# Kernel optimization log

Hardware: AMD Instinct MI355X
Metric: run time of the kernel (lower is better)

## Reference

```python
import jax, jax.numpy as jnp
import numpy as np

BN_EPS = 1e-3  # keras BatchNormalization default epsilon


def setup_inputs() -> dict:
    key = jax.random.key(0)
    ks = jax.random.split(key, 8)
    B, H, W, C, K, CLS = 8, 64, 64, 512, 32, 21
    std = 1.0 / (K * C) ** 0.5
    x = jax.random.normal(ks[0], (B, H, W, C), dtype=jnp.float32)
    codewords = jax.random.uniform(ks[1], (C, K), dtype=jnp.float32, minval=-std, maxval=std)
    smoothing_factors = jax.random.uniform(ks[2], (K,), dtype=jnp.float32, minval=-1.0, maxval=0.0)
    # BatchNormalization(axis=-2) over (B, features, K): per-feature params, inference stats
    bn_gamma = jnp.ones((C,), dtype=jnp.float32)
    bn_beta = jnp.zeros((C,), dtype=jnp.float32)
    bn_mean = jnp.zeros((C,), dtype=jnp.float32)
    bn_var = jnp.ones((C,), dtype=jnp.float32)
    # Dense layers (glorot-uniform style init)
    lim1 = (6.0 / (C + C)) ** 0.5
    w_enc = jax.random.uniform(ks[3], (C, C), dtype=jnp.float32, minval=-lim1, maxval=lim1)
    b_enc = jnp.zeros((C,), dtype=jnp.float32)
    lim2 = (6.0 / (C + CLS)) ** 0.5
    w_se = jax.random.uniform(ks[4], (C, CLS), dtype=jnp.float32, minval=-lim2, maxval=lim2)
    b_se = jnp.zeros((CLS,), dtype=jnp.float32)
    return {"x": x, "codewords": codewords, "smoothing_factors": smoothing_factors,
            "bn_gamma": bn_gamma, "bn_beta": bn_beta, "bn_mean": bn_mean, "bn_var": bn_var,
            "w_enc": w_enc, "b_enc": b_enc, "w_se": w_se, "b_se": b_se}


def _encoder(x, codewords, smoothing_factors, bn_gamma, bn_beta, bn_mean, bn_var):
    B, H, W, C = x.shape
    K = codewords.shape[1]
    N = H * W
    xf = x.reshape(B, N, C)
    # squared residual norms ||x_n - c_k||^2 via expansion (same math as the
    # explicit (B,N,C,K) residual tensor in the original, without materializing it)
    x_sq = jnp.sum(xf * xf, axis=-1, keepdims=True)          # (B,N,1)
    cw_sq = jnp.sum(codewords * codewords, axis=0)            # (K,)
    cross = jnp.einsum('bnc,ck->bnk', xf, codewords)          # (B,N,K)
    sqnorms = x_sq - 2.0 * cross + cw_sq                      # (B,N,K)
    # softmax over codewords of -(sqnorm * smoothing_factor)
    weights = jax.nn.softmax(-(sqnorms * smoothing_factors), axis=-1)  # (B,N,K)
    # sum_n w_nk * (x_n - c_k) = (w^T x)_ck - c_k * sum_n w_nk
    wx = jnp.einsum('bnk,bnc->bck', weights, xf)              # (B,C,K)
    wsum = jnp.sum(weights, axis=1)                           # (B,K)
    enc = wx - codewords[None, :, :] * wsum[:, None, :]       # (B,C,K)
    # BatchNorm(axis=-2) in inference mode: normalize per-feature across (B,K)
    inv = jax.lax.rsqrt(bn_var + BN_EPS)
    enc_bn = (enc - bn_mean[None, :, None]) * (inv * bn_gamma)[None, :, None] + bn_beta[None, :, None]
    enc_relu = jax.nn.relu(enc_bn)
    out = jnp.sum(enc_relu, axis=-1)                          # (B,C)
    return out.reshape(B, 1, 1, C)


def reference(x, codewords, smoothing_factors, bn_gamma, bn_beta, bn_mean, bn_var,
              w_enc, b_enc, w_se, b_se):
    B = x.shape[0]
    C = codewords.shape[0]
    encodings = _encoder(x, codewords, smoothing_factors, bn_gamma, bn_beta, bn_mean, bn_var)  # (B,1,1,C)
    attn = jax.nn.sigmoid(jnp.einsum('bijc,cd->bijd', encodings, w_enc) + b_enc)  # (B,1,1,C)
    featuremaps_output = attn * x                                                  # (B,H,W,C)
    enc_vec = encodings.reshape(B, C)
    se_loss_output = jax.nn.sigmoid(enc_vec @ w_se + b_se)                         # (B,classes)
    return featuremaps_output, se_loss_output
```

## Files before the change

### kernel.cpp

```cpp
#include <hip/hip_runtime.h>

#define BB 8
#define NN 4096
#define CCH 512
#define KK 32
#define CLS 21
#define BN_EPS 1e-3f

#define CHUNK 128
#define NBLK (NN / CHUNK)

typedef _Float16 f16;
typedef _Float16 f16x4 __attribute__((ext_vector_type(4)));
typedef _Float16 f16x8 __attribute__((ext_vector_type(8)));
typedef float f32x4 __attribute__((ext_vector_type(4)));

#define WP 136

#define WS_P    0
#define WS_WSP  (NBLK * BB * CCH * KK / 2)
#define WS_ENC  (WS_WSP + NBLK * BB * KK)
#define WS_END  (WS_ENC + BB * CCH)

template <int CTRL>
__device__ __forceinline__ float dpp_add(float v) {
    int r = __builtin_amdgcn_update_dpp(0, __builtin_bit_cast(int, v),
                                        CTRL, 0xF, 0xF, true);
    return v + __builtin_bit_cast(float, r);
}
template <int CTRL>
__device__ __forceinline__ float dpp_max(float v) {
    int r = __builtin_amdgcn_update_dpp(0, __builtin_bit_cast(int, v),
                                        CTRL, 0xF, 0xF, true);
    return fmaxf(v, __builtin_bit_cast(float, r));
}
__device__ __forceinline__ float rowsum16(float v) {
    v = dpp_add<0x128>(v); v = dpp_add<0x124>(v);
    v = dpp_add<0x122>(v); v = dpp_add<0x121>(v);
    return v;
}
__device__ __forceinline__ float rowmax16(float v) {
    v = dpp_max<0x128>(v); v = dpp_max<0x124>(v);
    v = dpp_max<0x122>(v); v = dpp_max<0x121>(v);
    return v;
}

__global__ __launch_bounds__(512, 2) void enc_mfma(
    const float* __restrict__ x, const float* __restrict__ cw,
    const float* __restrict__ sf, float* __restrict__ ws)
{
    __shared__ f16   cwL[2048 * 8];
    __shared__ f16   wexch[32 * WP];
    __shared__ float wsq[8][KK];
    __shared__ float csqL[KK];
    __shared__ float nsfL[KK];
    __shared__ float redtmp[8][KK];

    const int t = threadIdx.x;
    const int w = t >> 6, l = t & 63, a = l & 15, g = l >> 4;
    const int chunk = blockIdx.x, b = blockIdx.y;
    const int n0 = chunk * CHUNK;

#pragma unroll
    for (int si = 0; si < 4; ++si) {
        const int s     = si * 512 + t;
        const int lane  = s & 63;
        const int cstep = (s >> 6) & 15;
        const int kt    = s >> 10;
        const int k     = (lane & 15) + 16 * kt;
        const int c0    = cstep * 32 + (lane >> 4) * 8;
        f16x8 v;
#pragma unroll
        for (int i = 0; i < 8; ++i) v[i] = (f16)cw[(c0 + i) * KK + k];
        *reinterpret_cast<f16x8*>(cwL + (size_t)s * 8) = v;
    }
    if (t < 256) {
        const int k = t & 31, part = t >> 5;
        float s = 0.f;
        for (int c = part * 64; c < part * 64 + 64; ++c) {
            const float v = cw[c * KK + k];
            s += v * v;
        }
        redtmp[part][k] = s;
    }
    __syncthreads();
    if (t < KK) {
        float s = 0.f;
#pragma unroll
        for (int p = 0; p < 8; ++p) s += redtmp[p][t];
        csqL[t] = s;
        nsfL[t] = -sf[t];
    }
    __syncthreads();

    const float csq0 = csqL[a], csq1 = csqL[a + 16];
    const float nsf0 = nsfL[a], nsf1 = nsfL[a + 16];

    f32x4 d0 = {0.f, 0.f, 0.f, 0.f}, d1 = {0.f, 0.f, 0.f, 0.f};
    float xs = 0.f;
    {
        const float* xrow = x + (size_t)(b * NN + n0 + w * 16 + a) * CCH;
        float4 u0 = *reinterpret_cast<const float4*>(xrow + g * 8);
        float4 u1 = *reinterpret_cast<const float4*>(xrow + g * 8 + 4);
#pragma unroll
        for (int cs = 0; cs < 16; ++cs) {
            float4 p0, p1;
            if (cs < 15) {
                const int cn = (cs + 1) * 32 + g * 8;
                p0 = *reinterpret_cast<const float4*>(xrow + cn);
                p1 = *reinterpret_cast<const float4*>(xrow + cn + 4);
            }
            xs += u0.x*u0.x + u0.y*u0.y + u0.z*u0.z + u0.w*u0.w
                + u1.x*u1.x + u1.y*u1.y + u1.z*u1.z + u1.w*u1.w;
            const f16x8 af = {(f16)u0.x, (f16)u0.y, (f16)u0.z, (f16)u0.w,
                              (f16)u1.x, (f16)u1.y, (f16)u1.z, (f16)u1.w};
            const f16x8 bf0 = *reinterpret_cast<const f16x8*>(
                cwL + ((size_t)cs * 64 + l) * 8);
            const f16x8 bf1 = *reinterpret_cast<const f16x8*>(
                cwL + ((size_t)(16 + cs) * 64 + l) * 8);
            d0 = __builtin_amdgcn_mfma_f32_16x16x32_f16(af, bf0, d0, 0, 0, 0);
            d1 = __builtin_amdgcn_mfma_f32_16x16x32_f16(af, bf1, d1, 0, 0, 0);
            u0 = p0; u1 = p1;
        }
        xs += __shfl_xor(xs, 16);
        xs += __shfl_xor(xs, 32);
    }

    float wsacc0 = 0.f, wsacc1 = 0.f;
#pragma unroll
    for (int r = 0; r < 4; ++r) {
        const int rho = g * 4 + r;
        const float xsr = __shfl(xs, rho);
        const float l0 = (xsr - 2.f * d0[r] + csq0) * nsf0;
        const float l1 = (xsr - 2.f * d1[r] + csq1) * nsf1;
        const float mx = rowmax16(fmaxf(l0, l1));
        const float e0 = __expf(l0 - mx);
        const float e1 = __expf(l1 - mx);
        const float inv = 1.f / rowsum16(e0 + e1);
        const float w0 = e0 * inv, w1 = e1 * inv;
        wsacc0 += w0; wsacc1 += w1;
        wexch[(a     ) * WP + w * 16 + rho] = (f16)w0;
        wexch[(a + 16) * WP + w * 16 + rho] = (f16)w1;
    }
    wsacc0 += __shfl_xor(wsacc0, 16); wsacc0 += __shfl_xor(wsacc0, 32);
    wsacc1 += __shfl_xor(wsacc1, 16); wsacc1 += __shfl_xor(wsacc1, 32);
    if (l < 16) { wsq[w][l] = wsacc0; wsq[w][l + 16] = wsacc1; }

    __syncthreads();

    f32x4 acc[4][2];
#pragma unroll
    for (int ct = 0; ct < 4; ++ct)
#pragma unroll
        for (int kt = 0; kt < 2; ++kt) acc[ct][kt] = (f32x4){0.f, 0.f, 0.f, 0.f};

    const int c0 = w * 64;
#pragma unroll
    for (int sq2 = 0; sq2 < 4; ++sq2) {
        const f16x8 a0 = *reinterpret_cast<const f16x8*>(
            &wexch[(a     ) * WP + sq2 * 32 + g * 8]);
        const f16x8 a1 = *reinterpret_cast<const f16x8*>(
            &wexch[(a + 16) * WP + sq2 * 32 + g * 8]);
        const float* xb = x + (size_t)(b * NN + n0 + sq2 * 32 + g * 8) * CCH;
#pragma unroll
        for (int ct = 0; ct < 4; ++ct) {
            const int c = c0 + ct * 16 + a;
            f16x8 B;
#pragma unroll
            for (int i = 0; i < 8; ++i) B[i] = (f16)xb[(size_t)i * CCH + c];
            acc[ct][0] = __builtin_amdgcn_mfma_f32_16x16x32_f16(a0, B, acc[ct][0], 0, 0, 0);
            acc[ct][1] = __builtin_amdgcn_mfma_f32_16x16x32_f16(a1, B, acc[ct][1], 0, 0, 0);
        }
    }

    {
        f16* pp = reinterpret_cast<f16*>(ws) +
                  ((size_t)(chunk * BB + b)) * CCH * KK;
#pragma unroll
        for (int ct = 0; ct < 4; ++ct) {
            const int c = c0 + ct * 16 + a;
#pragma unroll
            for (int kt = 0; kt < 2; ++kt) {
                const f32x4 v = acc[ct][kt];
                const f16x4 h = {(f16)v[0], (f16)v[1], (f16)v[2], (f16)v[3]};
                *reinterpret_cast<f16x4*>(
                    pp + (size_t)c * KK + kt * 16 + g * 4) = h;
            }
        }
    }
    if (t < KK) {
        float s = 0.f;
#pragma unroll
        for (int p = 0; p < 8; ++p) s += wsq[p][t];
        ws[WS_WSP + ((size_t)chunk * BB + b) * KK + t] = s;
    }
}

__global__ __launch_bounds__(256) void reduce_encv(
    float* __restrict__ ws, const float* __restrict__ cw,
    const float* __restrict__ gamma, const float* __restrict__ beta,
    const float* __restrict__ mean, const float* __restrict__ var)
{
    __shared__ float wsum_s[KK];
    const int b  = blockIdx.y;
    const int cs = blockIdx.x;
    const int t  = threadIdx.x;

    if (t < KK) {
        float s0 = 0.f, s1 = 0.f;
        for (int ch = 0; ch < NBLK; ch += 2) {
            s0 += ws[WS_WSP + ((size_t)(ch + 0) * BB + b) * KK + t];
            s1 += ws[WS_WSP + ((size_t)(ch + 1) * BB + b) * KK + t];
        }
        wsum_s[t] = s0 + s1;
    }
    __syncthreads();

    const int cl = t >> 3;
    const int c  = cs * 32 + cl;
    const int kq = t & 7;
    const f16* p = reinterpret_cast<const f16*>(ws) +
                   ((size_t)b * CCH + c) * KK + kq * 4;
    const size_t stride = (size_t)BB * CCH * KK;

    f32x4 a0 = {0.f, 0.f, 0.f, 0.f}, a1 = {0.f, 0.f, 0.f, 0.f};
    for (int ch = 0; ch < NBLK; ch += 2) {
        const f16x4 h0 = *reinterpret_cast<const f16x4*>(p + (ch + 0) * stride);
        const f16x4 h1 = *reinterpret_cast<const f16x4*>(p + (ch + 1) * stride);
        a0 += (f32x4){(float)h0[0], (float)h0[1], (float)h0[2], (float)h0[3]};
        a1 += (f32x4){(float)h1[0], (float)h1[1], (float)h1[2], (float)h1[3]};
    }
    const f32x4 aa = a0 + a1;

    const float g  = gamma[c] * rsqrtf(var[c] + BN_EPS);
    const float mu = mean[c];
    const float be = beta[c];
    const float4 cv = *reinterpret_cast<const float4*>(cw + c * KK + kq * 4);
    const float4 sv = *reinterpret_cast<const float4*>(&wsum_s[kq * 4]);
    float s = 0.f;
    s += fmaxf((aa[0] - cv.x * sv.x - mu) * g + be, 0.f);
    s += fmaxf((aa[1] - cv.y * sv.y - mu) * g + be, 0.f);
    s += fmaxf((aa[2] - cv.z * sv.z - mu) * g + be, 0.f);
    s += fmaxf((aa[3] - cv.w * sv.w - mu) * g + be, 0.f);
    s += __shfl_xor(s, 1);
    s += __shfl_xor(s, 2);
    s += __shfl_xor(s, 4);
    if (kq == 0) ws[WS_ENC + (size_t)b * CCH + c] = s;
}

__global__ __launch_bounds__(256) void scale_fused(
    const float* __restrict__ x, const float* __restrict__ enc,
    const float* __restrict__ w_enc, const float* __restrict__ b_enc,
    const float* __restrict__ w_se, const float* __restrict__ b_se,
    float* __restrict__ out)
{
    __shared__ float ev[CCH];
    __shared__ float red2[16][64];
    __shared__ float attnL[64];

    const int ns = blockIdx.x;
    const int cc = blockIdx.y;
    const int b  = blockIdx.z;
    const int t  = threadIdx.x;

    if (cc == 8) {
        if (ns != 0) return;
        ev[t]       = enc[(size_t)b * CCH + t];
        ev[t + 256] = enc[(size_t)b * CCH + 256 + t];
        __syncthreads();
        if (t < 8 * CLS) {
            const int j = t >> 3, p = t & 7;
            float a = 0.f;
            for (int c = p; c < CCH; c += 8) a += ev[c] * w_se[c * CLS + j];
            a += __shfl_xor(a, 1);
            a += __shfl_xor(a, 2);
            a += __shfl_xor(a, 4);
            if (p == 0)
                out[(size_t)BB * NN * CCH + b * CLS + j] =
                    1.f / (1.f + __expf(-(a + b_se[j])));
        }
        return;
    }

    ev[t]       = enc[(size_t)b * CCH + t];
    ev[t + 256] = enc[(size_t)b * CCH + 256 + t];
    __syncthreads();

    {
        const int quad = t & 15;
        const int p    = t >> 4;
        const float* wq = w_enc + (size_t)(p * 32) * CCH + cc * 64 + quad * 4;
        f32x4 q0 = {0.f, 0.f, 0.f, 0.f}, q1 = {0.f, 0.f, 0.f, 0.f};
        f32x4 q2 = {0.f, 0.f, 0.f, 0.f}, q3 = {0.f, 0.f, 0.f, 0.f};
#pragma unroll
        for (int i = 0; i < 32; i += 4) {
            const int c = p * 32 + i;
            q0 += ev[c + 0] * *reinterpret_cast<const f32x4*>(wq + (size_t)(i + 0) * CCH);
            q1 += ev[c + 1] * *reinterpret_cast<const f32x4*>(wq + (size_t)(i + 1) * CCH);
            q2 += ev[c + 2] * *reinterpret_cast<const f32x4*>(wq + (size_t)(i + 2) * CCH);
            q3 += ev[c + 3] * *reinterpret_cast<const f32x4*>(wq + (size_t)(i + 3) * CCH);
        }
        *reinterpret_cast<f32x4*>(&red2[p][quad * 4]) = (q0 + q1) + (q2 + q3);
        __syncthreads();
        if (t < 64) {
            float v = b_enc[cc * 64 + t];
#pragma unroll
            for (int p2 = 0; p2 < 16; ++p2) v += red2[p2][t];
            attnL[t] = 1.f / (1.f + __expf(-v));
        }
        __syncthreads();
    }

    const int q   = t & 15;
    const int rr0 = t >> 4;
    const f32x4 av = *reinterpret_cast<const f32x4*>(attnL + q * 4);
#pragma unroll 8
    for (int i = 0; i < 32; ++i) {
        const int r = ns * 512 + i * 16 + rr0;
        const size_t off = ((size_t)(b * NN + r)) * CCH + cc * 64 + q * 4;
        const f32x4 xv = *reinterpret_cast<const f32x4*>(x + off);
        __builtin_nontemporal_store(xv * av, reinterpret_cast<f32x4*>(out + off));
    }
}

extern "C" void kernel_launch(void* const* d_in, const int* in_sizes, int n_in,
                              void* d_out, int out_size, void* d_ws, size_t ws_size,
                              hipStream_t stream)
{
    const float* x     = (const float*)d_in[0];
    const float* cw    = (const float*)d_in[1];
    const float* sf    = (const float*)d_in[2];
    const float* gamma = (const float*)d_in[3];
    const float* beta  = (const float*)d_in[4];
    const float* mean  = (const float*)d_in[5];
    const float* var   = (const float*)d_in[6];
    const float* w_enc = (const float*)d_in[7];
    const float* b_enc = (const float*)d_in[8];
    const float* w_se  = (const float*)d_in[9];
    const float* b_se  = (const float*)d_in[10];
    float* out = (float*)d_out;
    float* ws  = (float*)d_ws;

    enc_mfma<<<dim3(NBLK, BB), 512, 0, stream>>>(x, cw, sf, ws);
    reduce_encv<<<dim3(16, BB), 256, 0, stream>>>(ws, cw, gamma, beta, mean, var);
    scale_fused<<<dim3(8, 9, BB), 256, 0, stream>>>(
        x, ws + WS_ENC, w_enc, b_enc, w_se, b_se, out);
}
```

Before: 60.26 us.

## Fuse encoder reduction into MFMA kernel via last-block atomic counter

```diff
diff --git a/kernel.cpp b/kernel.cpp
--- a/kernel.cpp
+++ b/kernel.cpp
@@ -20,7 +20,8 @@
 #define WS_P    0
 #define WS_WSP  (NBLK * BB * CCH * KK / 2)
 #define WS_ENC  (WS_WSP + NBLK * BB * KK)
-#define WS_END  (WS_ENC + BB * CCH)
+#define WS_CNT  (WS_ENC + BB * CCH)
+#define WS_END  (WS_CNT + BB)
 
 template <int CTRL>
 __device__ __forceinline__ float dpp_add(float v) {
@@ -47,7 +48,9 @@
 
 __global__ __launch_bounds__(512, 2) void enc_mfma(
     const float* __restrict__ x, const float* __restrict__ cw,
-    const float* __restrict__ sf, float* __restrict__ ws)
+    const float* __restrict__ sf, const float* __restrict__ gamma,
+    const float* __restrict__ beta, const float* __restrict__ mean,
+    const float* __restrict__ var, float* __restrict__ ws)
 {
     __shared__ f16   cwL[2048 * 8];
     __shared__ f16   wexch[32 * WP];
@@ -55,6 +58,7 @@
     __shared__ float csqL[KK];
     __shared__ float nsfL[KK];
     __shared__ float redtmp[8][KK];
+    __shared__ int   isLast;
 
     const int t = threadIdx.x;
     const int w = t >> 6, l = t & 63, a = l & 15, g = l >> 4;
@@ -194,58 +198,59 @@
         for (int p = 0; p < 8; ++p) s += wsq[p][t];
         ws[WS_WSP + ((size_t)chunk * BB + b) * KK + t] = s;
     }
-}
-
-__global__ __launch_bounds__(256) void reduce_encv(
-    float* __restrict__ ws, const float* __restrict__ cw,
-    const float* __restrict__ gamma, const float* __restrict__ beta,
-    const float* __restrict__ mean, const float* __restrict__ var)
-{
-    __shared__ float wsum_s[KK];
-    const int b  = blockIdx.y;
-    const int cs = blockIdx.x;
-    const int t  = threadIdx.x;
-
-    if (t < KK) {
-        float s0 = 0.f, s1 = 0.f;
-        for (int ch = 0; ch < NBLK; ch += 2) {
-            s0 += ws[WS_WSP + ((size_t)(ch + 0) * BB + b) * KK + t];
-            s1 += ws[WS_WSP + ((size_t)(ch + 1) * BB + b) * KK + t];
-        }
-        wsum_s[t] = s0 + s1;
-    }
-    __syncthreads();
-
-    const int cl = t >> 3;
-    const int c  = cs * 32 + cl;
-    const int kq = t & 7;
-    const f16* p = reinterpret_cast<const f16*>(ws) +
-                   ((size_t)b * CCH + c) * KK + kq * 4;
-    const size_t stride = (size_t)BB * CCH * KK;
-
-    f32x4 a0 = {0.f, 0.f, 0.f, 0.f}, a1 = {0.f, 0.f, 0.f, 0.f};
-    for (int ch = 0; ch < NBLK; ch += 2) {
-        const f16x4 h0 = *reinterpret_cast<const f16x4*>(p + (ch + 0) * stride);
-        const f16x4 h1 = *reinterpret_cast<const f16x4*>(p + (ch + 1) * stride);
-        a0 += (f32x4){(float)h0[0], (float)h0[1], (float)h0[2], (float)h0[3]};
-        a1 += (f32x4){(float)h1[0], (float)h1[1], (float)h1[2], (float)h1[3]};
-    }
-    const f32x4 aa = a0 + a1;
-
-    const float g  = gamma[c] * rsqrtf(var[c] + BN_EPS);
-    const float mu = mean[c];
-    const float be = beta[c];
-    const float4 cv = *reinterpret_cast<const float4*>(cw + c * KK + kq * 4);
-    const float4 sv = *reinterpret_cast<const float4*>(&wsum_s[kq * 4]);
-    float s = 0.f;
-    s += fmaxf((aa[0] - cv.x * sv.x - mu) * g + be, 0.f);
-    s += fmaxf((aa[1] - cv.y * sv.y - mu) * g + be, 0.f);
-    s += fmaxf((aa[2] - cv.z * sv.z - mu) * g + be, 0.f);
-    s += fmaxf((aa[3] - cv.w * sv.w - mu) * g + be, 0.f);
-    s += __shfl_xor(s, 1);
-    s += __shfl_xor(s, 2);
-    s += __shfl_xor(s, 4);
-    if (kq == 0) ws[WS_ENC + (size_t)b * CCH + c] = s;
+
+    __threadfence();
+    __syncthreads();
+    if (t == 0) {
+        unsigned* cnt = reinterpret_cast<unsigned*>(ws + WS_CNT);
+        const unsigned old = atomicAdd(&cnt[b], 1u);
+        isLast = (old == NBLK - 1);
+        if (isLast) cnt[b] = 0;
+    }
+    __syncthreads();
+    if (!isLast) return;
+    __threadfence();
+
+    {
+        if (t < KK) {
+            float s = 0.f;
+            for (int ch = 0; ch < NBLK; ++ch)
+                s += ws[WS_WSP + ((size_t)ch * BB + b) * KK + t];
+            redtmp[0][t] = s;
+        }
+        __syncthreads();
+
+        const int c = t;
+        const f16* p = reinterpret_cast<const f16*>(ws) +
+                       ((size_t)b * CCH + c) * KK;
+        const size_t stride = (size_t)BB * CCH * KK;
+
+        f32x4 aa[8];
+#pragma unroll
+        for (int q = 0; q < 8; ++q) aa[q] = (f32x4){0.f, 0.f, 0.f, 0.f};
+        for (int ch = 0; ch < NBLK; ++ch) {
+            const f16* pc = p + ch * stride;
+#pragma unroll
+            for (int q = 0; q < 8; ++q) {
+                const f16x4 h = *reinterpret_cast<const f16x4*>(pc + q * 4);
+                aa[q] += (f32x4){(float)h[0], (float)h[1], (float)h[2], (float)h[3]};
+            }
+        }
+        const float gk  = gamma[c] * rsqrtf(var[c] + BN_EPS);
+        const float mu = mean[c];
+        const float be = beta[c];
+        float s = 0.f;
+#pragma unroll
+        for (int q = 0; q < 8; ++q) {
+            const float4 cv = *reinterpret_cast<const float4*>(cw + c * KK + q * 4);
+            const float4 sv = *reinterpret_cast<const float4*>(&redtmp[0][q * 4]);
+            s += fmaxf((aa[q][0] - cv.x * sv.x - mu) * gk + be, 0.f);
+            s += fmaxf((aa[q][1] - cv.y * sv.y - mu) * gk + be, 0.f);
+            s += fmaxf((aa[q][2] - cv.z * sv.z - mu) * gk + be, 0.f);
+            s += fmaxf((aa[q][3] - cv.w * sv.w - mu) * gk + be, 0.f);
+        }
+        ws[WS_ENC + (size_t)b * CCH + c] = s;
+    }
 }
 
 __global__ __launch_bounds__(256) void scale_fused(
@@ -341,8 +346,10 @@
     float* out = (float*)d_out;
     float* ws  = (float*)d_ws;
 
-    enc_mfma<<<dim3(NBLK, BB), 512, 0, stream>>>(x, cw, sf, ws);
-    reduce_encv<<<dim3(16, BB), 256, 0, stream>>>(ws, cw, gamma, beta, mean, var);
+    hipMemsetAsync(ws + WS_CNT, 0, BB * sizeof(unsigned), stream);
+
+    enc_mfma<<<dim3(NBLK, BB), 512, 0, stream>>>(
+        x, cw, sf, gamma, beta, mean, var, ws);
     scale_fused<<<dim3(8, 9, BB), 256, 0, stream>>>(
         x, ws + WS_ENC, w_enc, b_enc, w_se, b_se, out);
 }
```

After: 147.6 us. +145.0%, slower.
